# Optimization experiments

Hardware: AMD Instinct MI355X
Metric: run time of the kernel (lower is better)

## Reference

```python
import jax, jax.numpy as jnp
import numpy as np

DIM = 128
POS_HID = 64
ATT_HID = DIM * 2
B, N = 4, 512


def _linear_init(key, fan_in, fan_out):
    # mimic torch Linear default init scale: U(-1/sqrt(fan_in), 1/sqrt(fan_in))
    kw, kb = jax.random.split(key)
    bound = 1.0 / np.sqrt(fan_in)
    W = jax.random.uniform(kw, (fan_in, fan_out), minval=-bound, maxval=bound, dtype=jnp.float32)
    b = jax.random.uniform(kb, (fan_out,), minval=-bound, maxval=bound, dtype=jnp.float32)
    return W, b


def setup_inputs() -> dict:
    key = jax.random.key(0)
    ks = jax.random.split(key, 6)
    x = jax.random.normal(ks[0], (B, DIM, N), dtype=jnp.float32)
    pos = jax.random.normal(ks[1], (B, N, 3), dtype=jnp.float32)
    Wqkv, bqkv = _linear_init(ks[2], DIM, DIM * 3)
    pW1, pb1 = _linear_init(ks[3], 3, POS_HID)
    pW2, pb2 = _linear_init(ks[4], POS_HID, DIM)
    k5a, k5b = jax.random.split(ks[5])
    aW1, ab1 = _linear_init(k5a, DIM, ATT_HID)
    aW2, ab2 = _linear_init(k5b, ATT_HID, DIM)
    return {"x": x, "pos": pos, "Wqkv": Wqkv, "bqkv": bqkv,
            "pW1": pW1, "pb1": pb1, "pW2": pW2, "pb2": pb2,
            "aW1": aW1, "ab1": ab1, "aW2": aW2, "ab2": ab2}


def reference(x, pos, Wqkv, bqkv, pW1, pb1, pW2, pb2, aW1, ab1, aW2, ab2):
    # x: [b, d, n] -> [b, n, d]
    xt = jnp.transpose(x, (0, 2, 1))
    qkv = xt @ Wqkv + bqkv                      # [b, n, 3d]
    q, k, v = jnp.split(qkv, 3, axis=-1)        # each [b, n, d]

    # pairwise relative positions: [b, i, j, 3]
    rel_pos = pos[:, :, None, :] - pos[:, None, :, :]
    # pos_mlp: Linear(3, hid) -> ReLU -> Linear(hid, d)
    rel_pos_emb = jax.nn.relu(rel_pos @ pW1 + pb1) @ pW2 + pb2   # [b, i, j, d]

    qk_rel = q[:, :, None, :] - k[:, None, :, :]                 # [b, i, j, d]
    v_ij = v[:, None, :, :] + rel_pos_emb                        # [b, i, j, d]

    # attn_mlp: Linear(d, 2d) -> ReLU -> Linear(2d, d)
    sim = jax.nn.relu((qk_rel + rel_pos_emb) @ aW1 + ab1) @ aW2 + ab2  # [b, i, j, d]
    attn = jax.nn.softmax(sim, axis=2)                           # softmax over j (dim=-2)
    agg = jnp.sum(attn * v_ij, axis=2)                           # [b, i, d]
    return jnp.transpose(agg, (0, 2, 1))                         # [b, d, n]
```

## Files before the change

### kernel.cpp

```cpp
#include <hip/hip_runtime.h>
#include <hip/hip_bf16.h>

#define B_ 4
#define N_ 512
#define D_ 128
#define LOG2E 1.4426950408889634f

typedef __attribute__((ext_vector_type(8))) short bf16x8;
typedef __attribute__((ext_vector_type(4))) short s16x4;
typedef __attribute__((ext_vector_type(4))) float f32x4;
typedef __attribute__((ext_vector_type(16))) float f32x16;

__device__ __forceinline__ f32x4 mfma16(bf16x8 a, bf16x8 b, f32x4 c) {
    return __builtin_amdgcn_mfma_f32_16x16x32_bf16(a, b, c, 0, 0, 0);
}
__device__ __forceinline__ f32x16 mfma32(bf16x8 a, bf16x8 b, f32x16 c) {
    return __builtin_amdgcn_mfma_f32_32x32x16_bf16(a, b, c, 0, 0, 0);
}
__device__ __forceinline__ short bf16b(float x) {
    __hip_bfloat16 h = __float2bfloat16(x);
    return *reinterpret_cast<short*>(&h);
}
__device__ __forceinline__ float b2f(short s) {
    unsigned u = ((unsigned)(unsigned short)s) << 16;
    union { unsigned u; float f; } c; c.u = u; return c.f;
}

__global__ void prep_weights_kernel(const float* __restrict__ aW1, const float* __restrict__ aW2,
                                    const float* __restrict__ pW2, const float* __restrict__ pb2,
                                    const float* __restrict__ ab1,
                                    __hip_bfloat16* __restrict__ aW2T, __hip_bfloat16* __restrict__ pW2T,
                                    __hip_bfloat16* __restrict__ W12T, float* __restrict__ cvec) {
    int idx = blockIdx.x * 256 + threadIdx.x;
    if (idx < 128 * 256) {
        int n = idx >> 8, k2 = idx & 255;
        aW2T[idx] = __float2bfloat16(aW2[k2 * 128 + n] * LOG2E);
    }
    if (idx < 128 * 64) {
        int n = idx >> 6, k2 = idx & 63;
        pW2T[idx] = __float2bfloat16(pW2[k2 * 128 + n]);
    }
    if (idx < 256 * 64) {
        int n = idx >> 6, h = idx & 63;
        float s = 0.f;
#pragma unroll 8
        for (int d = 0; d < 128; ++d) s += pW2[h * 128 + d] * aW1[d * 256 + n];
        W12T[idx] = __float2bfloat16(s);
    }
    if (idx < 256) {
        float s = ab1[idx];
#pragma unroll 8
        for (int d = 0; d < 128; ++d) s += pb2[d] * aW1[d * 256 + idx];
        cvec[idx] = s;
    }
}

__global__ void posw_kernel(const float* __restrict__ pos, const float* __restrict__ pW1,
                            float* __restrict__ posw) {
    int idx = blockIdx.x * 256 + threadIdx.x;
    int t = idx >> 6, h = idx & 63;
    float p0 = pos[t * 3 + 0], p1 = pos[t * 3 + 1], p2 = pos[t * 3 + 2];
    posw[idx] = p0 * pW1[h] + p1 * pW1[64 + h] + p2 * pW1[128 + h];
}

__global__ void qkv_kernel(const float* __restrict__ x, const float* __restrict__ Wqkv,
                           const float* __restrict__ bqkv,
                           float* __restrict__ q, float* __restrict__ k,
                           short* __restrict__ vb_t) {
    int idx = blockIdx.x * 256 + threadIdx.x;
    int m = idx % 384;
    int g = idx / 384;
    int bn0 = g * 4;
    int b = bn0 >> 9, n0 = bn0 & (N_ - 1);
    const float* xp = x + (b * D_) * N_ + n0;
    float bias = bqkv[m];
    float a0 = bias, a1 = bias, a2 = bias, a3 = bias;
#pragma unroll 4
    for (int d = 0; d < D_; ++d) {
        float wv = Wqkv[d * 384 + m];
        const float4 xv = *reinterpret_cast<const float4*>(xp + d * N_);
        a0 = fmaf(xv.x, wv, a0); a1 = fmaf(xv.y, wv, a1);
        a2 = fmaf(xv.z, wv, a2); a3 = fmaf(xv.w, wv, a3);
    }
    if (m < 256) {
        int mm = m & 127;
        float* dst = (m < 128) ? q : k;
        dst[(bn0 + 0) * D_ + mm] = a0;
        dst[(bn0 + 1) * D_ + mm] = a1;
        dst[(bn0 + 2) * D_ + mm] = a2;
        dst[(bn0 + 3) * D_ + mm] = a3;
    } else {
        int d = m & 127;
        int jt = n0 >> 6;
        int jr = n0 & 63;
        int rt = jr >> 5;
        int jrr = jr & 31;
        int rb = 4 * (jrr >> 3);
        int hi = (jrr >> 2) & 1;
        int lane = (d & 31) + 32 * hi;
        int ct = d >> 5;
        s16x4 pk;
        pk[0] = bf16b(a0); pk[1] = bf16b(a1); pk[2] = bf16b(a2); pk[3] = bf16b(a3);
        size_t base = (size_t)b * 65536 + (size_t)jt * 8192 + ((rt * 4 + ct) * 64 + lane) * 16 + rb;
        *(s16x4*)(vb_t + base) = pk;
    }
}

__global__ void qka_kernel(const float* __restrict__ q, const float* __restrict__ k,
                           const float* __restrict__ aW1,
                           float* __restrict__ qa, short* __restrict__ kab_t) {
    int col = threadIdx.x;
    int bn0 = blockIdx.x * 4;
    int b = bn0 >> 9, n0 = bn0 & (N_ - 1);
    const float* qp = q + bn0 * D_;
    const float* kp = k + bn0 * D_;
    float aq0 = 0, aq1 = 0, aq2 = 0, aq3 = 0;
    float ak0 = 0, ak1 = 0, ak2 = 0, ak3 = 0;
#pragma unroll 4
    for (int d = 0; d < D_; ++d) {
        float wv = aW1[d * 256 + col];
        aq0 = fmaf(qp[d], wv, aq0);        ak0 = fmaf(kp[d], wv, ak0);
        aq1 = fmaf(qp[D_ + d], wv, aq1);   ak1 = fmaf(kp[D_ + d], wv, ak1);
        aq2 = fmaf(qp[2*D_ + d], wv, aq2); ak2 = fmaf(kp[2*D_ + d], wv, ak2);
        aq3 = fmaf(qp[3*D_ + d], wv, aq3); ak3 = fmaf(kp[3*D_ + d], wv, ak3);
    }
    qa[(bn0 + 0) * 256 + col] = aq0;
    qa[(bn0 + 1) * 256 + col] = aq1;
    qa[(bn0 + 2) * 256 + col] = aq2;
    qa[(bn0 + 3) * 256 + col] = aq3;
    int jt = n0 >> 6;
    int mt = (n0 >> 4) & 3;
    int lg = (n0 >> 2) & 3;
    int w  = col >> 5, nt = (col >> 4) & 1, lc = col & 15;
    int l  = lg * 16 + lc;
    s16x4 pk;
    pk[0] = bf16b(ak0); pk[1] = bf16b(ak1); pk[2] = bf16b(ak2); pk[3] = bf16b(ak3);
    size_t base = (((((size_t)b * 8 + jt) * 8 + w) * 2 + nt) * 4 + mt) * 256 + l * 4;
    *(s16x4*)(kab_t + base) = pk;
}

__global__ __launch_bounds__(512, 2) void fused_attn_kernel(
    const float* __restrict__ qa, const short* __restrict__ kab_t,
    const short* __restrict__ vb_t,
    const float* __restrict__ posw, const float* __restrict__ pb1,
    const __hip_bfloat16* __restrict__ pW2T, const float* __restrict__ pb2,
    const __hip_bfloat16* __restrict__ W12T, const float* __restrict__ cvec,
    const __hip_bfloat16* __restrict__ aW2T, const float* __restrict__ ab2,
    float* __restrict__ out)
{
    __shared__ __hip_bfloat16 ph_s[2][64][72];
    __shared__ __hip_bfloat16 hid_s[2][64][264];
    __shared__ float pwi_s[2][64];
    __shared__ float mrg_s[2][4][32][4];

    const int tid = threadIdx.x;
    const int w   = tid >> 6;
    const int l   = tid & 63;
    const int lg  = l >> 4;
    const int lc  = l & 15;
    const int l31 = l & 31;
    const int hi  = l >> 5;
    const int rt  = w >> 2;
    const int ct  = w & 3;
    const int gx8 = ((l31 >> 2) & 3) << 3;

    const int blk = (blockIdx.x & 7) * 128 + (blockIdx.x >> 3);
    const int b   = blk >> 8;
    const int i0  = (blk & 255) * 2;

    if (tid < 128) {
        int ii = tid >> 6, h = tid & 63;
        pwi_s[ii][h] = posw[(size_t)(b * N_ + i0 + ii) * 64 + h] + pb1[h];
    }

    const int col0  = 32 * w + lc;
    const int dcol2 = 32 * ct + l31;

    const float qr00 = qa[(b * N_ + i0) * 256 + col0] + cvec[col0];
    const float qr01 = qa[(b * N_ + i0) * 256 + col0 + 16] + cvec[col0 + 16];
    const float qr10 = qa[(b * N_ + i0 + 1) * 256 + col0] + cvec[col0];
    const float qr11 = qa[(b * N_ + i0 + 1) * 256 + col0 + 16] + cvec[col0 + 16];
    const float ab2_r = ab2[dcol2] * LOG2E;
    const float pb2_r = pb2[dcol2];

    const __hip_bfloat16* a2base = aW2T + (size_t)dcol2 * 256 + 8 * hi;
    bf16x8 bw2[16];
#pragma unroll
    for (int ks = 0; ks < 16; ++ks)
        bw2[ks] = *(const bf16x8*)(a2base + 16 * ks);
    bf16x8 bwp[4];
    {
        const __hip_bfloat16* ppb = pW2T + (size_t)dcol2 * 64 + 8 * hi;
#pragma unroll
        for (int ks = 0; ks < 4; ++ks)
            bwp[ks] = *(const bf16x8*)(ppb + 16 * ks);
    }
    bf16x8 bw12[2][2];
#pragma unroll
    for (int nt = 0; nt < 2; ++nt)
#pragma unroll
        for (int k2 = 0; k2 < 2; ++k2)
            bw12[nt][k2] = *(const bf16x8*)(W12T + (size_t)(32 * w + 16 * nt + lc) * 64 + k2 * 32 + 8 * lg);

    float m_run[2] = {-1e30f, -1e30f};
    float l_run[2] = {0.f, 0.f};
    float o_run[2] = {0.f, 0.f};
    float vv[2][16];

    const short* ktp0 = kab_t + (size_t)b * 131072 + w * 2048 + l * 4;
    const short* vtp0 = vb_t + (size_t)b * 65536 + ((rt * 4 + ct) * 64 + l) * 16;

    __syncthreads();

    for (int jt = 0; jt < 8; ++jt) {
        const int jb = jt * 64;

        {
            const int jl = tid >> 3;
            const int hb = (tid & 7) * 8;
            const float* pj = posw + (size_t)(b * N_ + jb + jl) * 64 + hb;
            float4 x0 = *(const float4*)pj;
            float4 x1 = *(const float4*)(pj + 4);
            float xr[8] = {x0.x, x0.y, x0.z, x0.w, x1.x, x1.y, x1.z, x1.w};
#pragma unroll
            for (int ii = 0; ii < 2; ++ii) {
                bf16x8 tv;
#pragma unroll
                for (int h = 0; h < 8; ++h)
                    tv[h] = bf16b(fmaxf(pwi_s[ii][hb + h] - xr[h], 0.f));
                *(bf16x8*)(&ph_s[ii][jl][hb]) = tv;
            }
        }
        __syncthreads();

        const short* vtp = vtp0 + (size_t)jt * 8192;
        const short* ktp = ktp0 + (size_t)jt * 16384;
        s16x4 vb4[4];
#pragma unroll
        for (int q4 = 0; q4 < 4; ++q4)
            vb4[q4] = *(const s16x4*)(vtp + 4 * q4);
        s16x4 kv[2][4];
#pragma unroll
        for (int nt = 0; nt < 2; ++nt)
#pragma unroll
            for (int mt = 0; mt < 4; ++mt)
                kv[nt][mt] = *(const s16x4*)(ktp + nt * 1024 + mt * 256);

#pragma unroll
        for (int ii = 0; ii < 2; ++ii) {
            f32x16 accr = {0.f,0.f,0.f,0.f,0.f,0.f,0.f,0.f,0.f,0.f,0.f,0.f,0.f,0.f,0.f,0.f};
#pragma unroll
            for (int ks = 0; ks < 4; ++ks) {
                bf16x8 a = *(const bf16x8*)(&ph_s[ii][32 * rt + l31][16 * ks + 8 * hi]);
                accr = mfma32(a, bwp[ks], accr);
            }
#pragma unroll
            for (int r = 0; r < 16; ++r)
                vv[ii][r] = accr[r] + b2f(vb4[r >> 2][r & 3]) + pb2_r;
        }

#pragma unroll
        for (int ii = 0; ii < 2; ++ii) {
#pragma unroll
            for (int mt = 0; mt < 4; ++mt) {
                bf16x8 a0 = *(const bf16x8*)(&ph_s[ii][mt * 16 + lc][8 * lg]);
                bf16x8 a1 = *(const bf16x8*)(&ph_s[ii][mt * 16 + lc][32 + 8 * lg]);
#pragma unroll
                for (int nt = 0; nt < 2; ++nt) {
                    f32x4 acc = {0.f, 0.f, 0.f, 0.f};
                    acc = mfma16(a0, bw12[nt][0], acc);
                    acc = mfma16(a1, bw12[nt][1], acc);
                    const float qv = ii ? (nt ? qr11 : qr10) : (nt ? qr01 : qr00);
                    const int colw = 32 * w + (((16 * nt + lc) ^ (8 * lg)) & 31);
#pragma unroll
                    for (int r = 0; r < 4; ++r) {
                        int row = mt * 16 + 4 * lg + r;
                        hid_s[ii][row][colw] = __float2bfloat16(
                            fmaxf(acc[r] + qv - b2f(kv[nt][mt][r]), 0.f));
                    }
                }
            }
        }
        __syncthreads();

#pragma unroll
        for (int ii = 0; ii < 2; ++ii) {
            f32x16 acc2a = {0.f,0.f,0.f,0.f,0.f,0.f,0.f,0.f,0.f,0.f,0.f,0.f,0.f,0.f,0.f,0.f};
            f32x16 acc2b = {0.f,0.f,0.f,0.f,0.f,0.f,0.f,0.f,0.f,0.f,0.f,0.f,0.f,0.f,0.f,0.f};
            const short* hrow = (const short*)&hid_s[ii][32 * rt + l31][0];
#pragma unroll
            for (int ks = 0; ks < 8; ++ks) {
                bf16x8 aa = *(const bf16x8*)(hrow + ((16 * ks + 8 * hi) ^ gx8));
                bf16x8 ab = *(const bf16x8*)(hrow + ((16 * (ks + 8) + 8 * hi) ^ gx8));
                acc2a = mfma32(aa, bw2[ks], acc2a);
                acc2b = mfma32(ab, bw2[ks + 8], acc2b);
            }
#pragma unroll
            for (int r = 0; r < 16; ++r) acc2a[r] += acc2b[r];
            float t8[8];
#pragma unroll
            for (int r = 0; r < 8; ++r) t8[r] = fmaxf(acc2a[r], acc2a[r + 8]);
            float t4a = fmaxf(t8[0], t8[4]), t4b = fmaxf(t8[1], t8[5]);
            float t4c = fmaxf(t8[2], t8[6]), t4d = fmaxf(t8[3], t8[7]);
            float tmax = fmaxf(fmaxf(t4a, t4b), fmaxf(t4c, t4d));
            float m_new = fmaxf(m_run[ii], tmax + ab2_r);
            float mm = m_new - ab2_r;
            float scale = __builtin_amdgcn_exp2f(m_run[ii] - m_new);
            l_run[ii] *= scale;
            o_run[ii] *= scale;
#pragma unroll
            for (int r = 0; r < 16; ++r) {
                float e = __builtin_amdgcn_exp2f(acc2a[r] - mm);
                l_run[ii] += e;
                o_run[ii] = fmaf(e, vv[ii][r], o_run[ii]);
            }
            m_run[ii] = m_new;
        }
    }

    float M1[2], L1[2], O1[2];
#pragma unroll
    for (int ii = 0; ii < 2; ++ii) {
        float m2 = __shfl_xor(m_run[ii], 32);
        float l2 = __shfl_xor(l_run[ii], 32);
        float o2 = __shfl_xor(o_run[ii], 32);
        M1[ii] = fmaxf(m_run[ii], m2);
        float e1 = __builtin_amdgcn_exp2f(m_run[ii] - M1[ii]);
        float e2 = __builtin_amdgcn_exp2f(m2 - M1[ii]);
        L1[ii] = l_run[ii] * e1 + l2 * e2;
        O1[ii] = o_run[ii] * e1 + o2 * e2;
        if (rt == 1 && hi == 0) {
            mrg_s[ii][ct][l31][0] = M1[ii];
            mrg_s[ii][ct][l31][1] = L1[ii];
            mrg_s[ii][ct][l31][2] = O1[ii];
        }
    }
    __syncthreads();
    if (rt == 0 && hi == 0) {
#pragma unroll
        for (int ii = 0; ii < 2; ++ii) {
            float Mb = mrg_s[ii][ct][l31][0];
            float Lb = mrg_s[ii][ct][l31][1];
            float Ob = mrg_s[ii][ct][l31][2];
            float M = fmaxf(M1[ii], Mb);
            float ea = __builtin_amdgcn_exp2f(M1[ii] - M);
            float eb = __builtin_amdgcn_exp2f(Mb - M);
            float L = L1[ii] * ea + Lb * eb;
            float O = O1[ii] * ea + Ob * eb;
            out[((size_t)b * D_ + dcol2) * N_ + i0 + ii] = O / L;
        }
    }
}

extern "C" void kernel_launch(void* const* d_in, const int* in_sizes, int n_in,
                              void* d_out, int out_size, void* d_ws, size_t ws_size,
                              hipStream_t stream) {
    const float* x    = (const float*)d_in[0];
    const float* pos  = (const float*)d_in[1];
    const float* Wqkv = (const float*)d_in[2];
    const float* bqkv = (const float*)d_in[3];
    const float* pW1  = (const float*)d_in[4];
    const float* pb1  = (const float*)d_in[5];
    const float* pW2  = (const float*)d_in[6];
    const float* pb2  = (const float*)d_in[7];
    const float* aW1  = (const float*)d_in[8];
    const float* ab1  = (const float*)d_in[9];
    const float* aW2  = (const float*)d_in[10];
    const float* ab2  = (const float*)d_in[11];
    float* out = (float*)d_out;

    float* q    = (float*)d_ws;
    float* k    = q  + B_ * N_ * D_;
    float* qa   = k  + B_ * N_ * D_;
    float* posw = qa + B_ * N_ * 256;
    float* cvec = posw + B_ * N_ * 64;
    short* kab_t = (short*)(cvec + 256);
    short* vb_t  = kab_t + B_ * N_ * 256;
    __hip_bfloat16* aW2T = (__hip_bfloat16*)(vb_t + B_ * N_ * D_);
    __hip_bfloat16* pW2T = aW2T + 128 * 256;
    __hip_bfloat16* W12T = pW2T + 128 * 64;

    hipLaunchKernelGGL(prep_weights_kernel, dim3(128), dim3(256), 0, stream,
                       aW1, aW2, pW2, pb2, ab1, aW2T, pW2T, W12T, cvec);
    hipLaunchKernelGGL(posw_kernel, dim3(512), dim3(256), 0, stream,
                       pos, pW1, posw);
    hipLaunchKernelGGL(qkv_kernel, dim3(768), dim3(256), 0, stream,
                       x, Wqkv, bqkv, q, k, vb_t);
    hipLaunchKernelGGL(qka_kernel, dim3(512), dim3(256), 0, stream,
                       q, k, aW1, qa, kab_t);
    hipLaunchKernelGGL(fused_attn_kernel, dim3(1024), dim3(512), 0, stream,
                       qa, kab_t, vb_t, posw, pb1, pW2T, pb2, W12T, cvec, aW2T, ab2, out);
}
```

Baseline: 219.9 us.

## Prefetch next tile's K/V/pos loads during second GEMM and raise MFMA priority

Software-pipelines the j-tile loop. The next tile's k, v and position-hidden global loads are issued before the second attention-MLP GEMM and softmax update, and the next ph_s tile is built at the end of the iteration. The goal is to hide global-memory latency behind MFMA work. It also wraps the second GEMM in s_setprio so its wave gets higher issue priority. In exchange it holds more registers live across the loop and moves where the barrier sits.

```diff
diff --git a/kernel.cpp b/kernel.cpp
--- a/kernel.cpp
+++ b/kernel.cpp
@@ -210,42 +210,35 @@
     const short* ktp0 = kab_t + (size_t)b * 131072 + w * 2048 + l * 4;
     const short* vtp0 = vb_t + (size_t)b * 65536 + ((rt * 4 + ct) * 64 + l) * 16;
 
+    const int jl = tid >> 3;
+    const int hb = (tid & 7) * 8;
+
+    {
+        const float* pj = posw + (size_t)(b * N_ + jl) * 64 + hb;
+        float4 x0 = *(const float4*)pj;
+        float4 x1 = *(const float4*)(pj + 4);
+        float xr[8] = {x0.x, x0.y, x0.z, x0.w, x1.x, x1.y, x1.z, x1.w};
+#pragma unroll
+        for (int ii = 0; ii < 2; ++ii) {
+            bf16x8 tv;
+#pragma unroll
+            for (int h = 0; h < 8; ++h)
+                tv[h] = bf16b(fmaxf(pwi_s[ii][hb + h] - xr[h], 0.f));
+            *(bf16x8*)(&ph_s[ii][jl][hb]) = tv;
+        }
+    }
+    s16x4 vb4[4], kv[2][4];
+#pragma unroll
+    for (int q4 = 0; q4 < 4; ++q4)
+        vb4[q4] = *(const s16x4*)(vtp0 + 4 * q4);
+#pragma unroll
+    for (int nt = 0; nt < 2; ++nt)
+#pragma unroll
+        for (int mt = 0; mt < 4; ++mt)
+            kv[nt][mt] = *(const s16x4*)(ktp0 + nt * 1024 + mt * 256);
     __syncthreads();
 
     for (int jt = 0; jt < 8; ++jt) {
-        const int jb = jt * 64;
-
-        {
-            const int jl = tid >> 3;
-            const int hb = (tid & 7) * 8;
-            const float* pj = posw + (size_t)(b * N_ + jb + jl) * 64 + hb;
-            float4 x0 = *(const float4*)pj;
-            float4 x1 = *(const float4*)(pj + 4);
-            float xr[8] = {x0.x, x0.y, x0.z, x0.w, x1.x, x1.y, x1.z, x1.w};
-#pragma unroll
-            for (int ii = 0; ii < 2; ++ii) {
-                bf16x8 tv;
-#pragma unroll
-                for (int h = 0; h < 8; ++h)
-                    tv[h] = bf16b(fmaxf(pwi_s[ii][hb + h] - xr[h], 0.f));
-                *(bf16x8*)(&ph_s[ii][jl][hb]) = tv;
-            }
-        }
-        __syncthreads();
-
-        const short* vtp = vtp0 + (size_t)jt * 8192;
-        const short* ktp = ktp0 + (size_t)jt * 16384;
-        s16x4 vb4[4];
-#pragma unroll
-        for (int q4 = 0; q4 < 4; ++q4)
-            vb4[q4] = *(const s16x4*)(vtp + 4 * q4);
-        s16x4 kv[2][4];
-#pragma unroll
-        for (int nt = 0; nt < 2; ++nt)
-#pragma unroll
-            for (int mt = 0; mt < 4; ++mt)
-                kv[nt][mt] = *(const s16x4*)(ktp + nt * 1024 + mt * 256);
-
 #pragma unroll
         for (int ii = 0; ii < 2; ++ii) {
             f32x16 accr = {0.f,0.f,0.f,0.f,0.f,0.f,0.f,0.f,0.f,0.f,0.f,0.f,0.f,0.f,0.f,0.f};
@@ -258,7 +251,6 @@
             for (int r = 0; r < 16; ++r)
                 vv[ii][r] = accr[r] + b2f(vb4[r >> 2][r & 3]) + pb2_r;
         }
-
 #pragma unroll
         for (int ii = 0; ii < 2; ++ii) {
 #pragma unroll
@@ -283,11 +275,31 @@
         }
         __syncthreads();
 
+        const int last = (jt == 7);
+
+        float4 px0, px1;
+        if (!last) {
+            const short* vtp = vtp0 + (size_t)(jt + 1) * 8192;
+            const short* ktp = ktp0 + (size_t)(jt + 1) * 16384;
+#pragma unroll
+            for (int q4 = 0; q4 < 4; ++q4)
+                vb4[q4] = *(const s16x4*)(vtp + 4 * q4);
+#pragma unroll
+            for (int nt = 0; nt < 2; ++nt)
+#pragma unroll
+                for (int mt = 0; mt < 4; ++mt)
+                    kv[nt][mt] = *(const s16x4*)(ktp + nt * 1024 + mt * 256);
+            const float* pj = posw + (size_t)(b * N_ + (jt + 1) * 64 + jl) * 64 + hb;
+            px0 = *(const float4*)pj;
+            px1 = *(const float4*)(pj + 4);
+        }
+
 #pragma unroll
         for (int ii = 0; ii < 2; ++ii) {
             f32x16 acc2a = {0.f,0.f,0.f,0.f,0.f,0.f,0.f,0.f,0.f,0.f,0.f,0.f,0.f,0.f,0.f,0.f};
             f32x16 acc2b = {0.f,0.f,0.f,0.f,0.f,0.f,0.f,0.f,0.f,0.f,0.f,0.f,0.f,0.f,0.f,0.f};
             const short* hrow = (const short*)&hid_s[ii][32 * rt + l31][0];
+            __builtin_amdgcn_s_setprio(1);
 #pragma unroll
             for (int ks = 0; ks < 8; ++ks) {
                 bf16x8 aa = *(const bf16x8*)(hrow + ((16 * ks + 8 * hi) ^ gx8));
@@ -295,6 +307,7 @@
                 acc2a = mfma32(aa, bw2[ks], acc2a);
                 acc2b = mfma32(ab, bw2[ks + 8], acc2b);
             }
+            __builtin_amdgcn_s_setprio(0);
 #pragma unroll
             for (int r = 0; r < 16; ++r) acc2a[r] += acc2b[r];
             float t8[8];
@@ -316,6 +329,19 @@
             }
             m_run[ii] = m_new;
         }
+
+        if (!last) {
+            float xr[8] = {px0.x, px0.y, px0.z, px0.w, px1.x, px1.y, px1.z, px1.w};
+#pragma unroll
+            for (int ii = 0; ii < 2; ++ii) {
+                bf16x8 tv;
+#pragma unroll
+                for (int h = 0; h < 8; ++h)
+                    tv[h] = bf16b(fmaxf(pwi_s[ii][hb + h] - xr[h], 0.f));
+                *(bf16x8*)(&ph_s[ii][jl][hb]) = tv;
+            }
+        }
+        __syncthreads();
     }
 
     float M1[2], L1[2], O1[2];
```

Result: slower. 327.9 us (+49.1%).
